# Performance work log

Hardware: AMD Instinct MI355X
Metric: run time of the kernel (lower is better)

The kernel has to match this reference:

```python
import jax, jax.numpy as jnp
import numpy as np

B, N, D = 8, 4096, 6          # clouds, points per cloud, coordinate dim
K = 64                        # max_num_neighbors in radius query
NS1, NS2 = 2048, 512          # fps ratios 0.5 and 0.25
R1, R2 = 0.2, 0.4             # ball-query radii
DIMS = {1: [6, 64, 64, 128], 2: [134, 128, 128, 256], 3: [262, 256, 512, 1024], 4: [1024, 512, 512]}


def setup_inputs():
    key = jax.random.key(0)
    k0, k1, k2 = jax.random.split(key, 3)
    inp = {}
    inp['synapse_cordi'] = jax.random.normal(k0, (B * N, D), jnp.float32)
    inp['batch_index'] = jnp.repeat(jnp.arange(B, dtype=jnp.int32), N)
    inp['weight'] = jax.random.uniform(k1, (B * N,), jnp.float32)
    k = k2
    for i, dims in DIMS.items():
        for j in range(len(dims) - 1):
            k, kw = jax.random.split(k)
            inp[f'w{i}_{j}'] = jax.random.normal(kw, (dims[j], dims[j + 1]), jnp.float32) * (1.0 / float(np.sqrt(dims[j])))
            inp[f'b{i}_{j}'] = jnp.zeros((dims[j + 1],), jnp.float32)
    return inp


def _mlp(x, params):
    # PyG MLP, plain_last=True; batch-norm at default (eval, running stats) is identity
    n = len(params)
    for i, (W, b) in enumerate(params):
        x = x @ W + b
        if i < n - 1:
            x = jax.nn.relu(x)
    return x


def _fps(pos, n_s):
    # farthest point sampling on one cloud [N, D] -> [n_s] indices (deterministic start at 0)
    d0 = jnp.sum((pos - pos[0]) ** 2, axis=-1)
    def step(mind, _):
        nxt = jnp.argmax(mind)
        mind = jnp.minimum(mind, jnp.sum((pos - pos[nxt]) ** 2, axis=-1))
        return mind, nxt
    _, idxs = jax.lax.scan(step, d0, None, length=n_s - 1)
    return jnp.concatenate([jnp.zeros((1,), idxs.dtype), idxs])


def _ball(pos, pos_q, r):
    # radius query: up to K nearest points within r for each query; [n_q,K] idx + validity mask
    d2 = jnp.sum((pos_q[:, None, :] - pos[None, :, :]) ** 2, axis=-1)  # [n_q, N]
    neg = jnp.where(d2 <= r * r, -d2, -jnp.inf)
    vals, nbr = jax.lax.top_k(neg, K)
    return nbr, vals > -jnp.inf


def _sa(x, pos, params, n_s, r):
    # Weight_Sample_Module: fps -> radius -> PointNetConv (gather, MLP, masked max-scatter)
    idx = jax.vmap(lambda p: _fps(p, n_s))(pos)                     # [B, n_s]
    pos_q = jnp.take_along_axis(pos, idx[..., None], axis=1)        # [B, n_s, D]
    nbr, valid = jax.vmap(lambda p, q: _ball(p, q, r))(pos, pos_q)  # [B, n_s, K]
    gather = lambda a: jax.vmap(lambda t, i: t[i])(a, nbr)          # [B, n_s, K, C]
    rel = gather(pos) - pos_q[:, :, None, :]
    feat = rel if x is None else jnp.concatenate([gather(x), rel], axis=-1)
    h = _mlp(feat, params)                                          # [B, n_s, K, C_out]
    h = jnp.where(valid[..., None], h, -jnp.inf)
    return jnp.max(h, axis=2), pos_q                                # max aggregation


def reference(synapse_cordi, batch_index, weight,
              w1_0, b1_0, w1_1, b1_1, w1_2, b1_2,
              w2_0, b2_0, w2_1, b2_1, w2_2, b2_2,
              w3_0, b3_0, w3_1, b3_1, w3_2, b3_2,
              w4_0, b4_0, w4_1, b4_1):
    pos = synapse_cordi.reshape(B, N, D)  # uniform clouds; batch_index = repeat(arange(B), N)
    p1 = [(w1_0, b1_0), (w1_1, b1_1), (w1_2, b1_2)]
    p2 = [(w2_0, b2_0), (w2_1, b2_1), (w2_2, b2_2)]
    p3 = [(w3_0, b3_0), (w3_1, b3_1), (w3_2, b3_2)]
    p4 = [(w4_0, b4_0), (w4_1, b4_1)]
    x1, pos1 = _sa(None, pos, p1, NS1, R1)   # [B, 2048, 128]
    x2, pos2 = _sa(x1, pos1, p2, NS2, R2)    # [B, 512, 256]
    h = _mlp(jnp.concatenate([x2, pos2], axis=-1), p3)  # [B, 512, 1024]
    g = jnp.max(h, axis=1)                   # global max pool -> [B, 1024]
    return _mlp(g, p4)                       # [B, 512]
```

## Files before the change

kernel.cpp:

```cpp
#include <hip/hip_runtime.h>
#include <math.h>

#define B_ 8
#define N_ 4096
#define D_ 6
#define K_ 64
#define NS1_ 2048
#define NS2_ 512

typedef float v2f __attribute__((ext_vector_type(2)));


__device__ __forceinline__ float dist2_rn(const float* __restrict__ a, const float* __restrict__ q) {
    float s = 0.f;
#pragma unroll
    for (int d = 0; d < 6; ++d) {
        float diff = __fsub_rn(a[d], q[d]);
        s = __fadd_rn(s, __fmul_rn(diff, diff));
    }
    return s;
}

__device__ __forceinline__ unsigned mapf(float x) {
    unsigned u = __float_as_uint(x);
    return (u & 0x80000000u) ? ~u : (u | 0x80000000u);
}
__device__ __forceinline__ float unmapf(unsigned u) {
    return __uint_as_float((u & 0x80000000u) ? (u & 0x7FFFFFFFu) : ~u);
}

template <int CTRL>
__device__ __forceinline__ double dppd(double k) {
    int lo = __double2loint(k), hi = __double2hiint(k);
    int nlo = __builtin_amdgcn_update_dpp(lo, lo, CTRL, 0xF, 0xF, false);
    int nhi = __builtin_amdgcn_update_dpp(hi, hi, CTRL, 0xF, 0xF, false);
    return __hiloint2double(nhi, nlo);
}


__device__ __forceinline__ void wait_flag(unsigned* f, int t) {
    if (t == 0) {
        while (__hip_atomic_load(f, __ATOMIC_RELAXED, __HIP_MEMORY_SCOPE_AGENT) == 0u)
            __builtin_amdgcn_s_sleep(32);
        __builtin_amdgcn_fence(__ATOMIC_ACQUIRE, "agent");
    }
    __syncthreads();
}


template <int NP, int NS>
__device__ __forceinline__ void fps_core(float* __restrict__ spos, int* __restrict__ sidx,
                                         double* __restrict__ part, int t) {
#pragma clang fp contract(off)
    constexpr int NT = 256;
    constexpr int P = NP / NT;
    constexpr int HP = P / 2;
    int lane = t & 63, w = t >> 6;

    v2f px2[HP][6];
#pragma unroll
    for (int j = 0; j < HP; ++j)
#pragma unroll
        for (int d = 0; d < 6; ++d) {
            px2[j][d].x = spos[(t + NT * (2 * j)) * 6 + d];
            px2[j][d].y = spos[(t + NT * (2 * j + 1)) * 6 + d];
        }

    float cx[6];
#pragma unroll
    for (int d = 0; d < 6; ++d) cx[d] = spos[d];

    v2f mind2[HP];
    float runv = -1.f;
    int runj = 0;
#pragma unroll
    for (int j = 0; j < HP; ++j) {
        v2f d2 = {0.f, 0.f};
#pragma unroll
        for (int d = 0; d < 6; ++d) {
            v2f df = px2[j][d] - cx[d];
            d2 = d2 + df * df;
        }
        mind2[j] = d2;
        if (d2.x > runv) { runv = d2.x; runj = t + NT * (2 * j); }
        if (d2.y > runv) { runv = d2.y; runj = t + NT * (2 * j + 1); }
    }

    for (int s = 1; s < NS; ++s) {
        double key = __hiloint2double((int)__float_as_uint(runv), (int)(unsigned)(~runj));
        key = fmax(key, dppd<0x111>(key));
        key = fmax(key, dppd<0x112>(key));
        key = fmax(key, dppd<0x114>(key));
        key = fmax(key, dppd<0x118>(key));
        key = fmax(key, dppd<0x142>(key));
        key = fmax(key, dppd<0x143>(key));
        if (lane == 63) part[(s & 1) * 4 + w] = key;
        __syncthreads();
        double kk = part[(s & 1) * 4 + (lane & 3)];
        kk = fmax(kk, dppd<0x111>(kk));
        kk = fmax(kk, dppd<0x112>(kk));
        int nx = ~__builtin_amdgcn_readlane(__double2loint(kk), 3);
        if (t == 0) sidx[s] = nx;

        const float2* sv2 = (const float2*)spos;
        float2 ca = sv2[nx * 3], cb = sv2[nx * 3 + 1], cc = sv2[nx * 3 + 2];
        cx[0] = ca.x; cx[1] = ca.y; cx[2] = cb.x; cx[3] = cb.y; cx[4] = cc.x; cx[5] = cc.y;

        runv = -1.f;
        runj = 0;
#pragma unroll
        for (int j = 0; j < HP; ++j) {
            v2f d2 = {0.f, 0.f};
#pragma unroll
            for (int d = 0; d < 6; ++d) {
                v2f df = px2[j][d] - cx[d];
                d2 = d2 + df * df;
            }
            float mx = fminf(mind2[j].x, d2.x);
            float my = fminf(mind2[j].y, d2.y);
            mind2[j].x = mx;
            mind2[j].y = my;
            if (mx > runv) { runv = mx; runj = t + NT * (2 * j); }
            if (my > runv) { runv = my; runj = t + NT * (2 * j + 1); }
        }
    }
}


template <int NPTS, int S>
__device__ __forceinline__ int ball_scan(const float* __restrict__ sp,
                                         const float* __restrict__ posq,
                                         float r2, int qid, int tid,
                                         float* __restrict__ sd, unsigned short* __restrict__ si) {
    float q[6];
#pragma unroll
    for (int d = 0; d < 6; ++d) q[d] = posq[(size_t)qid * 6 + d];

    int n = 0;
    float thr = INFINITY;
#pragma unroll 4
    for (int j = 0; j < NPTS; ++j) {
        float d2 = dist2_rn(sp + j * 6, q);
        if (d2 <= r2 && (n < K_ || d2 < thr)) {
            int i = (n < K_) ? n : (K_ - 1);
            if (n < K_) ++n;
            while (i > 0 && sd[(i - 1) * S + tid] > d2) {
                sd[i * S + tid] = sd[(i - 1) * S + tid];
                si[i * S + tid] = si[(i - 1) * S + tid];
                --i;
            }
            sd[i * S + tid] = d2;
            si[i * S + tid] = (unsigned short)j;
            if (n == K_) thr = sd[(K_ - 1) * S + tid];
        }
    }
    return n;
}


__global__ __launch_bounds__(256, 1) void stage12_kernel(
        const float* __restrict__ pos, float* __restrict__ pos1, float* __restrict__ pos2,
        float* __restrict__ x1, int* __restrict__ nbr2, int* __restrict__ cnt2,
        unsigned* __restrict__ g, unsigned* flags,
        const float* __restrict__ W1_0, const float* __restrict__ B1_0,
        const float* __restrict__ W1_1, const float* __restrict__ B1_1,
        const float* __restrict__ W1_2, const float* __restrict__ B1_2,
        float r2_1, float r2_2) {
    __shared__ union Smem {
        struct { float spos[N_ * 6]; int sidx[NS1_]; double part[8]; } fps;
        struct { float spos[N_ * 6]; float sd[K_ * 128]; unsigned short si[K_ * 128];
                 unsigned short scnt[128]; } p1;
        struct { float spos1[NS1_ * 6]; float sd2[K_ * 64]; unsigned short si2[K_ * 64]; } b2;
    } sm;
    int t = threadIdx.x;
    int lane = t & 63, w = t >> 6;

    if (blockIdx.x < 8) {
        int b = blockIdx.x;
        float* spos = sm.fps.spos;
        int* sidx = sm.fps.sidx;
        double* part = sm.fps.part;

        {
            const float4* src = (const float4*)(pos + (size_t)b * N_ * 6);
            float4* dst = (float4*)spos;
            for (int e = t; e < N_ * 6 / 4; e += 256) dst[e] = src[e];
        }
        if (t == 0) sidx[0] = 0;
        __syncthreads();

        fps_core<N_, NS1_>(spos, sidx, part, t);
        __syncthreads();

        float smp[NS1_ / 256][6];
#pragma unroll
        for (int i = 0; i < NS1_ / 256; ++i) {
            int s = t + 256 * i;
            int ix = sidx[s];
#pragma unroll
            for (int d = 0; d < 6; ++d) smp[i][d] = spos[ix * 6 + d];
        }
#pragma unroll
        for (int i = 0; i < NS1_ / 256; ++i) {
            int s = t + 256 * i;
#pragma unroll
            for (int d = 0; d < 6; ++d) pos1[((size_t)b * NS1_ + s) * 6 + d] = smp[i][d];
        }
        __syncthreads();
        if (t == 0) {
            __threadfence();
            __hip_atomic_store(&flags[b], 1u, __ATOMIC_RELEASE, __HIP_MEMORY_SCOPE_AGENT);
        }

#pragma unroll
        for (int i = 0; i < NS1_ / 256; ++i) {
            int s = t + 256 * i;
#pragma unroll
            for (int d = 0; d < 6; ++d) spos[s * 6 + d] = smp[i][d];
        }
        for (int e = t; e < 1024; e += 256) g[b * 1024 + e] = 0u;
        if (t == 0) sidx[0] = 0;
        __syncthreads();

        fps_core<NS1_, NS2_>(spos, sidx, part, t);
        __syncthreads();

        for (int s = t; s < NS2_; s += 256) {
            int ix = sidx[s];
#pragma unroll
            for (int d = 0; d < 6; ++d) pos2[((size_t)b * NS2_ + s) * 6 + d] = spos[ix * 6 + d];
        }
        __syncthreads();
        if (t == 0) {
            __threadfence();
            __hip_atomic_store(&flags[8 + b], 1u, __ATOMIC_RELEASE, __HIP_MEMORY_SCOPE_AGENT);
        }
    } else if (blockIdx.x < 8 + 128) {
        int blk = blockIdx.x - 8;
        int b = blk >> 4;
        {
            const float4* src = (const float4*)(pos + (size_t)b * N_ * 6);
            float4* dst = (float4*)sm.p1.spos;
            for (int e = t; e < N_ * 6 / 4; e += 256) dst[e] = src[e];
        }
        __syncthreads();
        wait_flag(&flags[b], t);

        int qbase1 = b * NS1_ + (blk & 15) * 128;
        if (t < 128) {
            int n = ball_scan<N_, 128>(sm.p1.spos, pos1, r2_1, qbase1 + t, t, sm.p1.sd, sm.p1.si);
            sm.p1.scnt[t] = (unsigned short)n;
        }
        __syncthreads();

        for (int qq = 0; qq < 32; ++qq) {
            int lq = w * 32 + qq;
            int qid = qbase1 + lq;
            float q[6];
#pragma unroll
            for (int d = 0; d < 6; ++d) q[d] = pos1[(size_t)qid * 6 + d];
            int c = sm.p1.scnt[lq];
            float m0 = -INFINITY, m1 = -INFINITY;
            for (int n = 0; n < c; ++n) {
                int j = sm.p1.si[n * 128 + lq];
                float rel[6];
#pragma unroll
                for (int d = 0; d < 6; ++d) rel[d] = sm.p1.spos[j * 6 + d] - q[d];
                float a = B1_0[lane];
#pragma unroll
                for (int d = 0; d < 6; ++d) a = fmaf(W1_0[d * 64 + lane], rel[d], a);
                float h1 = fmaxf(a, 0.f);
                float a2 = B1_1[lane];
                for (int k = 0; k < 64; ++k) {
                    float v = __shfl(h1, k, 64);
                    a2 = fmaf(W1_1[k * 64 + lane], v, a2);
                }
                float h2 = fmaxf(a2, 0.f);
                float o0 = B1_2[lane], o1 = B1_2[64 + lane];
                for (int k = 0; k < 64; ++k) {
                    float v = __shfl(h2, k, 64);
                    o0 = fmaf(W1_2[k * 128 + lane], v, o0);
                    o1 = fmaf(W1_2[k * 128 + 64 + lane], v, o1);
                }
                m0 = fmaxf(m0, o0);
                m1 = fmaxf(m1, o1);
            }
            x1[(size_t)qid * 128 + lane] = m0;
            x1[(size_t)qid * 128 + 64 + lane] = m1;
        }
    } else {
        int blk = blockIdx.x - 136;
        int b = blk >> 3;
        wait_flag(&flags[b], t);
        {
            const float4* src = (const float4*)(pos1 + (size_t)b * NS1_ * 6);
            float4* dst = (float4*)sm.b2.spos1;
            for (int e = t; e < NS1_ * 6 / 4; e += 256) dst[e] = src[e];
        }
        __syncthreads();
        wait_flag(&flags[8 + b], t);
        if (t < 64) {
            int qid = blk * 64 + t;
            int n = ball_scan<NS1_, 64>(sm.b2.spos1, pos2, r2_2, qid, t, sm.b2.sd2, sm.b2.si2);
            cnt2[qid] = n;
            for (int i = 0; i < n; ++i) nbr2[(size_t)qid * K_ + i] = (int)sm.b2.si2[i * 64 + t];
        }
    }
}


__global__ __launch_bounds__(256, 1) void sa2_mlp3_kernel(
        const float* __restrict__ pos1, const float* __restrict__ pos2,
        const int* __restrict__ nbr, const int* __restrict__ cnt,
        const float* __restrict__ x1,
        const float* __restrict__ W1, const float* __restrict__ B1,
        const float* __restrict__ W2, const float* __restrict__ B2,
        const float* __restrict__ W3, const float* __restrict__ B3,
        const float* __restrict__ M0, const float* __restrict__ MB0,
        const float* __restrict__ M1, const float* __restrict__ MB1,
        const float* __restrict__ M2, const float* __restrict__ MB2,
        unsigned* __restrict__ g) {
    __shared__ float sx2[16 * 256];
    int lane = threadIdx.x & 63;
    int w = threadIdx.x >> 6;
    int qbase = blockIdx.x * 16;
    int b = qbase >> 9;

    for (int qq = 0; qq < 4; ++qq) {
        int lq = w * 4 + qq;
        int qid = qbase + lq;
        float q[6];
#pragma unroll
        for (int d = 0; d < 6; ++d) q[d] = pos2[(size_t)qid * 6 + d];
        int c = cnt[qid];
        float m0 = -INFINITY, m1 = -INFINITY, m2 = -INFINITY, m3 = -INFINITY;
        for (int n = 0; n < c; ++n) {
            int j = nbr[(size_t)qid * K_ + n];
            size_t row = (size_t)b * NS1_ + j;
            const float* xs = x1 + row * 128;
            float rel[6];
#pragma unroll
            for (int d = 0; d < 6; ++d) rel[d] = pos1[row * 6 + d] - q[d];
            float a0e = B1[lane], a0o = 0.f, a1e = B1[64 + lane], a1o = 0.f;
            for (int k = 0; k < 128; k += 2) {
                float v0 = xs[k], v1 = xs[k + 1];
                a0e = fmaf(W1[k * 128 + lane], v0, a0e);
                a1e = fmaf(W1[k * 128 + 64 + lane], v0, a1e);
                a0o = fmaf(W1[(k + 1) * 128 + lane], v1, a0o);
                a1o = fmaf(W1[(k + 1) * 128 + 64 + lane], v1, a1o);
            }
            float a0 = a0e + a0o, a1 = a1e + a1o;
#pragma unroll
            for (int d = 0; d < 6; ++d) {
                float v = rel[d];
                a0 = fmaf(W1[(128 + d) * 128 + lane], v, a0);
                a1 = fmaf(W1[(128 + d) * 128 + 64 + lane], v, a1);
            }
            float h1a = fmaxf(a0, 0.f), h1b = fmaxf(a1, 0.f);
            float c0 = B2[lane], c1 = B2[64 + lane];
            for (int k = 0; k < 64; ++k) {
                float v = __shfl(h1a, k, 64);
                c0 = fmaf(W2[k * 128 + lane], v, c0);
                c1 = fmaf(W2[k * 128 + 64 + lane], v, c1);
            }
            for (int k = 0; k < 64; ++k) {
                float v = __shfl(h1b, k, 64);
                c0 = fmaf(W2[(64 + k) * 128 + lane], v, c0);
                c1 = fmaf(W2[(64 + k) * 128 + 64 + lane], v, c1);
            }
            float h2a = fmaxf(c0, 0.f), h2b = fmaxf(c1, 0.f);
            float e0 = B3[lane], e1 = B3[64 + lane], e2 = B3[128 + lane], e3 = B3[192 + lane];
            for (int k = 0; k < 64; ++k) {
                float v = __shfl(h2a, k, 64);
                e0 = fmaf(W3[k * 256 + lane], v, e0);
                e1 = fmaf(W3[k * 256 + 64 + lane], v, e1);
                e2 = fmaf(W3[k * 256 + 128 + lane], v, e2);
                e3 = fmaf(W3[k * 256 + 192 + lane], v, e3);
            }
            for (int k = 0; k < 64; ++k) {
                float v = __shfl(h2b, k, 64);
                e0 = fmaf(W3[(64 + k) * 256 + lane], v, e0);
                e1 = fmaf(W3[(64 + k) * 256 + 64 + lane], v, e1);
                e2 = fmaf(W3[(64 + k) * 256 + 128 + lane], v, e2);
                e3 = fmaf(W3[(64 + k) * 256 + 192 + lane], v, e3);
            }
            m0 = fmaxf(m0, e0);
            m1 = fmaxf(m1, e1);
            m2 = fmaxf(m2, e2);
            m3 = fmaxf(m3, e3);
        }
        sx2[lq * 256 + lane] = m0;
        sx2[lq * 256 + 64 + lane] = m1;
        sx2[lq * 256 + 128 + lane] = m2;
        sx2[lq * 256 + 192 + lane] = m3;
    }
    __syncthreads();

    int lq0 = w * 4;
    int qid0 = qbase + lq0;

    float xr[4][4];
#pragma unroll
    for (int q = 0; q < 4; ++q)
#pragma unroll
        for (int j = 0; j < 4; ++j) xr[q][j] = sx2[(lq0 + q) * 256 + j * 64 + lane];

    float a[4][4];
    {
        float4 bv = *(const float4*)&MB0[lane * 4];
#pragma unroll
        for (int q = 0; q < 4; ++q) { a[q][0] = bv.x; a[q][1] = bv.y; a[q][2] = bv.z; a[q][3] = bv.w; }
    }
#pragma unroll
    for (int j = 0; j < 4; ++j) {
        for (int k2 = 0; k2 < 64; ++k2) {
            int k = j * 64 + k2;
            float4 wv = *(const float4*)&M0[(size_t)k * 256 + lane * 4];
#pragma unroll
            for (int q = 0; q < 4; ++q) {
                float v = __shfl(xr[q][j], k2, 64);
                a[q][0] = fmaf(wv.x, v, a[q][0]);
                a[q][1] = fmaf(wv.y, v, a[q][1]);
                a[q][2] = fmaf(wv.z, v, a[q][2]);
                a[q][3] = fmaf(wv.w, v, a[q][3]);
            }
        }
    }
#pragma unroll
    for (int d = 0; d < 6; ++d) {
        float4 wv = *(const float4*)&M0[(size_t)(256 + d) * 256 + lane * 4];
#pragma unroll
        for (int q = 0; q < 4; ++q) {
            float v = pos2[(size_t)(qid0 + q) * 6 + d];
            a[q][0] = fmaf(wv.x, v, a[q][0]);
            a[q][1] = fmaf(wv.y, v, a[q][1]);
            a[q][2] = fmaf(wv.z, v, a[q][2]);
            a[q][3] = fmaf(wv.w, v, a[q][3]);
        }
    }
    float h1[4][4];
#pragma unroll
    for (int q = 0; q < 4; ++q)
#pragma unroll
        for (int u = 0; u < 4; ++u) h1[q][u] = fmaxf(a[q][u], 0.f);

    float c[4][8];
    {
        float4 b0 = *(const float4*)&MB1[lane * 8];
        float4 b1 = *(const float4*)&MB1[lane * 8 + 4];
#pragma unroll
        for (int q = 0; q < 4; ++q) {
            c[q][0] = b0.x; c[q][1] = b0.y; c[q][2] = b0.z; c[q][3] = b0.w;
            c[q][4] = b1.x; c[q][5] = b1.y; c[q][6] = b1.z; c[q][7] = b1.w;
        }
    }
    for (int l = 0; l < 64; ++l) {
#pragma unroll
        for (int r = 0; r < 4; ++r) {
            int k = l * 4 + r;
            float4 w0 = *(const float4*)&M1[(size_t)k * 512 + lane * 8];
            float4 w1 = *(const float4*)&M1[(size_t)k * 512 + lane * 8 + 4];
#pragma unroll
            for (int q = 0; q < 4; ++q) {
                float v = __shfl(h1[q][r], l, 64);
                c[q][0] = fmaf(w0.x, v, c[q][0]);
                c[q][1] = fmaf(w0.y, v, c[q][1]);
                c[q][2] = fmaf(w0.z, v, c[q][2]);
                c[q][3] = fmaf(w0.w, v, c[q][3]);
                c[q][4] = fmaf(w1.x, v, c[q][4]);
                c[q][5] = fmaf(w1.y, v, c[q][5]);
                c[q][6] = fmaf(w1.z, v, c[q][6]);
                c[q][7] = fmaf(w1.w, v, c[q][7]);
            }
        }
    }
    float h2[4][8];
#pragma unroll
    for (int q = 0; q < 4; ++q)
#pragma unroll
        for (int u = 0; u < 8; ++u) h2[q][u] = fmaxf(c[q][u], 0.f);

    float e[4][16];
#pragma unroll
    for (int jj = 0; jj < 4; ++jj) {
        float4 bv = *(const float4*)&MB2[lane * 16 + jj * 4];
#pragma unroll
        for (int q = 0; q < 4; ++q) {
            e[q][jj * 4 + 0] = bv.x; e[q][jj * 4 + 1] = bv.y;
            e[q][jj * 4 + 2] = bv.z; e[q][jj * 4 + 3] = bv.w;
        }
    }
    for (int l = 0; l < 64; ++l) {
#pragma unroll
        for (int r = 0; r < 8; ++r) {
            int k = l * 8 + r;
            const float* wp = &M2[(size_t)k * 1024 + lane * 16];
            float4 w0 = *(const float4*)&wp[0];
            float4 w1 = *(const float4*)&wp[4];
            float4 w2 = *(const float4*)&wp[8];
            float4 w3 = *(const float4*)&wp[12];
#pragma unroll
            for (int q = 0; q < 4; ++q) {
                float v = __shfl(h2[q][r], l, 64);
                e[q][0]  = fmaf(w0.x, v, e[q][0]);
                e[q][1]  = fmaf(w0.y, v, e[q][1]);
                e[q][2]  = fmaf(w0.z, v, e[q][2]);
                e[q][3]  = fmaf(w0.w, v, e[q][3]);
                e[q][4]  = fmaf(w1.x, v, e[q][4]);
                e[q][5]  = fmaf(w1.y, v, e[q][5]);
                e[q][6]  = fmaf(w1.z, v, e[q][6]);
                e[q][7]  = fmaf(w1.w, v, e[q][7]);
                e[q][8]  = fmaf(w2.x, v, e[q][8]);
                e[q][9]  = fmaf(w2.y, v, e[q][9]);
                e[q][10] = fmaf(w2.z, v, e[q][10]);
                e[q][11] = fmaf(w2.w, v, e[q][11]);
                e[q][12] = fmaf(w3.x, v, e[q][12]);
                e[q][13] = fmaf(w3.y, v, e[q][13]);
                e[q][14] = fmaf(w3.z, v, e[q][14]);
                e[q][15] = fmaf(w3.w, v, e[q][15]);
            }
        }
    }
#pragma unroll
    for (int u = 0; u < 16; ++u) {
        float m = fmaxf(fmaxf(e[0][u], e[1][u]), fmaxf(e[2][u], e[3][u]));
        atomicMax(&g[b * 1024 + lane * 16 + u], mapf(m));
    }
}


__global__ __launch_bounds__(512) void mlp4_kernel(const unsigned* __restrict__ g,
                                                   const float* __restrict__ W0, const float* __restrict__ B0,
                                                   const float* __restrict__ W1, const float* __restrict__ B1,
                                                   float* __restrict__ out) {
    int b = blockIdx.x;
    int c = threadIdx.x;
    __shared__ float h[512];
    float a0 = B0[c], a1 = 0.f, a2 = 0.f, a3 = 0.f;
    for (int k = 0; k < 1024; k += 4) {
        float v0 = unmapf(g[b * 1024 + k]);
        float v1 = unmapf(g[b * 1024 + k + 1]);
        float v2 = unmapf(g[b * 1024 + k + 2]);
        float v3 = unmapf(g[b * 1024 + k + 3]);
        a0 = fmaf(v0, W0[k * 512 + c], a0);
        a1 = fmaf(v1, W0[(k + 1) * 512 + c], a1);
        a2 = fmaf(v2, W0[(k + 2) * 512 + c], a2);
        a3 = fmaf(v3, W0[(k + 3) * 512 + c], a3);
    }
    h[c] = fmaxf((a0 + a1) + (a2 + a3), 0.f);
    __syncthreads();
    float o0 = B1[c], o1 = 0.f, o2 = 0.f, o3 = 0.f;
    for (int k = 0; k < 512; k += 4) {
        o0 = fmaf(h[k], W1[k * 512 + c], o0);
        o1 = fmaf(h[k + 1], W1[(k + 1) * 512 + c], o1);
        o2 = fmaf(h[k + 2], W1[(k + 2) * 512 + c], o2);
        o3 = fmaf(h[k + 3], W1[(k + 3) * 512 + c], o3);
    }
    out[(size_t)b * 512 + c] = (o0 + o1) + (o2 + o3);
}


extern "C" void kernel_launch(void* const* d_in, const int* in_sizes, int n_in,
                              void* d_out, int out_size, void* d_ws, size_t ws_size,
                              hipStream_t stream) {
    const float* pos = (const float*)d_in[0];
    const float* w1_0 = (const float*)d_in[3];
    const float* b1_0 = (const float*)d_in[4];
    const float* w1_1 = (const float*)d_in[5];
    const float* b1_1 = (const float*)d_in[6];
    const float* w1_2 = (const float*)d_in[7];
    const float* b1_2 = (const float*)d_in[8];
    const float* w2_0 = (const float*)d_in[9];
    const float* b2_0 = (const float*)d_in[10];
    const float* w2_1 = (const float*)d_in[11];
    const float* b2_1 = (const float*)d_in[12];
    const float* w2_2 = (const float*)d_in[13];
    const float* b2_2 = (const float*)d_in[14];
    const float* w3_0 = (const float*)d_in[15];
    const float* b3_0 = (const float*)d_in[16];
    const float* w3_1 = (const float*)d_in[17];
    const float* b3_1 = (const float*)d_in[18];
    const float* w3_2 = (const float*)d_in[19];
    const float* b3_2 = (const float*)d_in[20];
    const float* w4_0 = (const float*)d_in[21];
    const float* b4_0 = (const float*)d_in[22];
    const float* w4_1 = (const float*)d_in[23];
    const float* b4_1 = (const float*)d_in[24];
    float* out = (float*)d_out;

    char* ws = (char*)d_ws;
    size_t off = 0;
    float* pos1 = (float*)(ws + off);    off += (size_t)B_ * NS1_ * 6 * 4;
    float* pos2 = (float*)(ws + off);    off += (size_t)B_ * NS2_ * 6 * 4;
    float* x1 = (float*)(ws + off);      off += (size_t)B_ * NS1_ * 128 * 4;
    int* nbr2 = (int*)(ws + off);        off += (size_t)B_ * NS2_ * K_ * 4;
    int* cnt2 = (int*)(ws + off);        off += (size_t)B_ * NS2_ * 4;
    unsigned* g = (unsigned*)(ws + off); off += (size_t)B_ * 1024 * 4;
    unsigned* flags = (unsigned*)(ws + off); off += 16 * 4;

    const float r2_1 = (float)(0.2 * 0.2);
    const float r2_2 = (float)(0.4 * 0.4);

    hipMemsetAsync(flags, 0, 16 * 4, stream);

    stage12_kernel<<<200, 256, 0, stream>>>(pos, pos1, pos2, x1, nbr2, cnt2, g, flags,
                                            w1_0, b1_0, w1_1, b1_1, w1_2, b1_2,
                                            r2_1, r2_2);
    sa2_mlp3_kernel<<<(B_ * NS2_) / 16, 256, 0, stream>>>(pos1, pos2, nbr2, cnt2, x1,
                                                          w2_0, b2_0, w2_1, b2_1, w2_2, b2_2,
                                                          w3_0, b3_0, w3_1, b3_1, w3_2, b3_2, g);
    mlp4_kernel<<<B_, 512, 0, stream>>>(g, w4_0, b4_0, w4_1, b4_1, out);
}
```

Before: 2.498 ms.

## Split SA2 conv from MLP3 and stage MLP3 weights in double-buffered LDS

Splits the fused SA2+MLP3 kernel in two. The new SA2 conv kernel handles 4 queries per block without the occupancy-1 bound, so it can launch 1024 blocks instead of 256, and it writes x2 to a global workspace. A separate MLP3 kernel reads x2 and streams the M1/M2 weight rows through double-buffered shared memory, replacing per-lane global loads. This adds an extra kernel launch, an x2 round-trip through global memory, and two block barriers per k-step in MLP3.

```diff
diff --git a/kernel.cpp b/kernel.cpp
--- a/kernel.cpp
+++ b/kernel.cpp
@@ -309,101 +309,103 @@
 }
 
 
-__global__ __launch_bounds__(256, 1) void sa2_mlp3_kernel(
-        const float* __restrict__ pos1, const float* __restrict__ pos2,
-        const int* __restrict__ nbr, const int* __restrict__ cnt,
-        const float* __restrict__ x1,
-        const float* __restrict__ W1, const float* __restrict__ B1,
-        const float* __restrict__ W2, const float* __restrict__ B2,
-        const float* __restrict__ W3, const float* __restrict__ B3,
-        const float* __restrict__ M0, const float* __restrict__ MB0,
-        const float* __restrict__ M1, const float* __restrict__ MB1,
-        const float* __restrict__ M2, const float* __restrict__ MB2,
-        unsigned* __restrict__ g) {
-    __shared__ float sx2[16 * 256];
+__global__ __launch_bounds__(256) void sa2_conv(const float* __restrict__ pos1, const float* __restrict__ posq,
+                                                const int* __restrict__ nbr, const int* __restrict__ cnt,
+                                                const float* __restrict__ x1,
+                                                const float* __restrict__ W1, const float* __restrict__ B1,
+                                                const float* __restrict__ W2, const float* __restrict__ B2,
+                                                const float* __restrict__ W3, const float* __restrict__ B3,
+                                                float* __restrict__ out) {
     int lane = threadIdx.x & 63;
     int w = threadIdx.x >> 6;
-    int qbase = blockIdx.x * 16;
-    int b = qbase >> 9;
-
-    for (int qq = 0; qq < 4; ++qq) {
-        int lq = w * 4 + qq;
-        int qid = qbase + lq;
-        float q[6];
-#pragma unroll
-        for (int d = 0; d < 6; ++d) q[d] = pos2[(size_t)qid * 6 + d];
-        int c = cnt[qid];
-        float m0 = -INFINITY, m1 = -INFINITY, m2 = -INFINITY, m3 = -INFINITY;
-        for (int n = 0; n < c; ++n) {
-            int j = nbr[(size_t)qid * K_ + n];
-            size_t row = (size_t)b * NS1_ + j;
-            const float* xs = x1 + row * 128;
-            float rel[6];
-#pragma unroll
-            for (int d = 0; d < 6; ++d) rel[d] = pos1[row * 6 + d] - q[d];
-            float a0e = B1[lane], a0o = 0.f, a1e = B1[64 + lane], a1o = 0.f;
-            for (int k = 0; k < 128; k += 2) {
-                float v0 = xs[k], v1 = xs[k + 1];
-                a0e = fmaf(W1[k * 128 + lane], v0, a0e);
-                a1e = fmaf(W1[k * 128 + 64 + lane], v0, a1e);
-                a0o = fmaf(W1[(k + 1) * 128 + lane], v1, a0o);
-                a1o = fmaf(W1[(k + 1) * 128 + 64 + lane], v1, a1o);
-            }
-            float a0 = a0e + a0o, a1 = a1e + a1o;
-#pragma unroll
-            for (int d = 0; d < 6; ++d) {
-                float v = rel[d];
-                a0 = fmaf(W1[(128 + d) * 128 + lane], v, a0);
-                a1 = fmaf(W1[(128 + d) * 128 + 64 + lane], v, a1);
-            }
-            float h1a = fmaxf(a0, 0.f), h1b = fmaxf(a1, 0.f);
-            float c0 = B2[lane], c1 = B2[64 + lane];
-            for (int k = 0; k < 64; ++k) {
-                float v = __shfl(h1a, k, 64);
-                c0 = fmaf(W2[k * 128 + lane], v, c0);
-                c1 = fmaf(W2[k * 128 + 64 + lane], v, c1);
-            }
-            for (int k = 0; k < 64; ++k) {
-                float v = __shfl(h1b, k, 64);
-                c0 = fmaf(W2[(64 + k) * 128 + lane], v, c0);
-                c1 = fmaf(W2[(64 + k) * 128 + 64 + lane], v, c1);
-            }
-            float h2a = fmaxf(c0, 0.f), h2b = fmaxf(c1, 0.f);
-            float e0 = B3[lane], e1 = B3[64 + lane], e2 = B3[128 + lane], e3 = B3[192 + lane];
-            for (int k = 0; k < 64; ++k) {
-                float v = __shfl(h2a, k, 64);
-                e0 = fmaf(W3[k * 256 + lane], v, e0);
-                e1 = fmaf(W3[k * 256 + 64 + lane], v, e1);
-                e2 = fmaf(W3[k * 256 + 128 + lane], v, e2);
-                e3 = fmaf(W3[k * 256 + 192 + lane], v, e3);
-            }
-            for (int k = 0; k < 64; ++k) {
-                float v = __shfl(h2b, k, 64);
-                e0 = fmaf(W3[(64 + k) * 256 + lane], v, e0);
-                e1 = fmaf(W3[(64 + k) * 256 + 64 + lane], v, e1);
-                e2 = fmaf(W3[(64 + k) * 256 + 128 + lane], v, e2);
-                e3 = fmaf(W3[(64 + k) * 256 + 192 + lane], v, e3);
-            }
-            m0 = fmaxf(m0, e0);
-            m1 = fmaxf(m1, e1);
-            m2 = fmaxf(m2, e2);
-            m3 = fmaxf(m3, e3);
-        }
-        sx2[lq * 256 + lane] = m0;
-        sx2[lq * 256 + 64 + lane] = m1;
-        sx2[lq * 256 + 128 + lane] = m2;
-        sx2[lq * 256 + 192 + lane] = m3;
-    }
-    __syncthreads();
-
-    int lq0 = w * 4;
-    int qid0 = qbase + lq0;
+    int qid = blockIdx.x * 4 + w;
+    int b = qid / NS2_;
+    float q[6];
+#pragma unroll
+    for (int d = 0; d < 6; ++d) q[d] = posq[(size_t)qid * 6 + d];
+    int c = cnt[qid];
+    float m0 = -INFINITY, m1 = -INFINITY, m2 = -INFINITY, m3 = -INFINITY;
+
+    for (int n = 0; n < c; ++n) {
+        int j = nbr[(size_t)qid * K_ + n];
+        size_t row = (size_t)b * NS1_ + j;
+        const float* xs = x1 + row * 128;
+        float rel[6];
+#pragma unroll
+        for (int d = 0; d < 6; ++d) rel[d] = pos1[row * 6 + d] - q[d];
+        float a0e = B1[lane], a0o = 0.f, a1e = B1[64 + lane], a1o = 0.f;
+        for (int k = 0; k < 128; k += 2) {
+            float v0 = xs[k], v1 = xs[k + 1];
+            a0e = fmaf(W1[k * 128 + lane], v0, a0e);
+            a1e = fmaf(W1[k * 128 + 64 + lane], v0, a1e);
+            a0o = fmaf(W1[(k + 1) * 128 + lane], v1, a0o);
+            a1o = fmaf(W1[(k + 1) * 128 + 64 + lane], v1, a1o);
+        }
+        float a0 = a0e + a0o, a1 = a1e + a1o;
+#pragma unroll
+        for (int d = 0; d < 6; ++d) {
+            float v = rel[d];
+            a0 = fmaf(W1[(128 + d) * 128 + lane], v, a0);
+            a1 = fmaf(W1[(128 + d) * 128 + 64 + lane], v, a1);
+        }
+        float h1a = fmaxf(a0, 0.f), h1b = fmaxf(a1, 0.f);
+        float c0 = B2[lane], c1 = B2[64 + lane];
+        for (int k = 0; k < 64; ++k) {
+            float v = __shfl(h1a, k, 64);
+            c0 = fmaf(W2[k * 128 + lane], v, c0);
+            c1 = fmaf(W2[k * 128 + 64 + lane], v, c1);
+        }
+        for (int k = 0; k < 64; ++k) {
+            float v = __shfl(h1b, k, 64);
+            c0 = fmaf(W2[(64 + k) * 128 + lane], v, c0);
+            c1 = fmaf(W2[(64 + k) * 128 + 64 + lane], v, c1);
+        }
+        float h2a = fmaxf(c0, 0.f), h2b = fmaxf(c1, 0.f);
+        float e0 = B3[lane], e1 = B3[64 + lane], e2 = B3[128 + lane], e3 = B3[192 + lane];
+        for (int k = 0; k < 64; ++k) {
+            float v = __shfl(h2a, k, 64);
+            e0 = fmaf(W3[k * 256 + lane], v, e0);
+            e1 = fmaf(W3[k * 256 + 64 + lane], v, e1);
+            e2 = fmaf(W3[k * 256 + 128 + lane], v, e2);
+            e3 = fmaf(W3[k * 256 + 192 + lane], v, e3);
+        }
+        for (int k = 0; k < 64; ++k) {
+            float v = __shfl(h2b, k, 64);
+            e0 = fmaf(W3[(64 + k) * 256 + lane], v, e0);
+            e1 = fmaf(W3[(64 + k) * 256 + 64 + lane], v, e1);
+            e2 = fmaf(W3[(64 + k) * 256 + 128 + lane], v, e2);
+            e3 = fmaf(W3[(64 + k) * 256 + 192 + lane], v, e3);
+        }
+        m0 = fmaxf(m0, e0);
+        m1 = fmaxf(m1, e1);
+        m2 = fmaxf(m2, e2);
+        m3 = fmaxf(m3, e3);
+    }
+    out[(size_t)qid * 256 + lane] = m0;
+    out[(size_t)qid * 256 + 64 + lane] = m1;
+    out[(size_t)qid * 256 + 128 + lane] = m2;
+    out[(size_t)qid * 256 + 192 + lane] = m3;
+}
+
+
+__global__ __launch_bounds__(256, 1) void mlp3_kernel(const float* __restrict__ x2, const float* __restrict__ pos2,
+                                                      const float* __restrict__ M0, const float* __restrict__ MB0,
+                                                      const float* __restrict__ M1w, const float* __restrict__ MB1,
+                                                      const float* __restrict__ M2w, const float* __restrict__ MB2,
+                                                      unsigned* __restrict__ g) {
+    __shared__ alignas(16) float sM1[2][4 * 512];
+    __shared__ alignas(16) float sM2[2][8 * 1024];
+    int t = threadIdx.x;
+    int lane = t & 63;
+    int w = t >> 6;
+    int qid0 = blockIdx.x * 16 + w * 4;
+    int b = qid0 >> 9;
 
     float xr[4][4];
 #pragma unroll
     for (int q = 0; q < 4; ++q)
 #pragma unroll
-        for (int j = 0; j < 4; ++j) xr[q][j] = sx2[(lq0 + q) * 256 + j * 64 + lane];
+        for (int j = 0; j < 4; ++j) xr[q][j] = x2[(size_t)(qid0 + q) * 256 + j * 64 + lane];
 
     float a[4][4];
     {
@@ -454,12 +456,25 @@
             c[q][4] = b1.x; c[q][5] = b1.y; c[q][6] = b1.z; c[q][7] = b1.w;
         }
     }
+    {
+        const float4* src = (const float4*)M1w;
+        float4* dst = (float4*)sM1[0];
+        dst[t] = src[t];
+        dst[t + 256] = src[t + 256];
+    }
+    __syncthreads();
     for (int l = 0; l < 64; ++l) {
+        int cur = l & 1;
+        float4 rg0, rg1;
+        if (l < 63) {
+            const float4* src = (const float4*)&M1w[(size_t)(l + 1) * 2048];
+            rg0 = src[t];
+            rg1 = src[t + 256];
+        }
 #pragma unroll
         for (int r = 0; r < 4; ++r) {
-            int k = l * 4 + r;
-            float4 w0 = *(const float4*)&M1[(size_t)k * 512 + lane * 8];
-            float4 w1 = *(const float4*)&M1[(size_t)k * 512 + lane * 8 + 4];
+            float4 w0 = *(const float4*)&sM1[cur][r * 512 + lane * 8];
+            float4 w1 = *(const float4*)&sM1[cur][r * 512 + lane * 8 + 4];
 #pragma unroll
             for (int q = 0; q < 4; ++q) {
                 float v = __shfl(h1[q][r], l, 64);
@@ -473,6 +488,13 @@
                 c[q][7] = fmaf(w1.w, v, c[q][7]);
             }
         }
+        __syncthreads();
+        if (l < 63) {
+            float4* dst = (float4*)sM1[cur ^ 1];
+            dst[t] = rg0;
+            dst[t + 256] = rg1;
+        }
+        __syncthreads();
     }
     float h2[4][8];
 #pragma unroll
@@ -490,11 +512,24 @@
             e[q][jj * 4 + 2] = bv.z; e[q][jj * 4 + 3] = bv.w;
         }
     }
+    {
+        const float4* src = (const float4*)M2w;
+        float4* dst = (float4*)sM2[0];
+#pragma unroll
+        for (int i = 0; i < 8; ++i) dst[t + 256 * i] = src[t + 256 * i];
+    }
+    __syncthreads();
     for (int l = 0; l < 64; ++l) {
+        int cur = l & 1;
+        float4 rg[8];
+        if (l < 63) {
+            const float4* src = (const float4*)&M2w[(size_t)(l + 1) * 8192];
+#pragma unroll
+            for (int i = 0; i < 8; ++i) rg[i] = src[t + 256 * i];
+        }
 #pragma unroll
         for (int r = 0; r < 8; ++r) {
-            int k = l * 8 + r;
-            const float* wp = &M2[(size_t)k * 1024 + lane * 16];
+            const float* wp = &sM2[cur][r * 1024 + lane * 16];
             float4 w0 = *(const float4*)&wp[0];
             float4 w1 = *(const float4*)&wp[4];
             float4 w2 = *(const float4*)&wp[8];
@@ -520,6 +555,13 @@
                 e[q][15] = fmaf(w3.w, v, e[q][15]);
             }
         }
+        __syncthreads();
+        if (l < 63) {
+            float4* dst = (float4*)sM2[cur ^ 1];
+#pragma unroll
+            for (int i = 0; i < 8; ++i) dst[t + 256 * i] = rg[i];
+        }
+        __syncthreads();
     }
 #pragma unroll
     for (int u = 0; u < 16; ++u) {
@@ -593,6 +635,7 @@
     float* pos1 = (float*)(ws + off);    off += (size_t)B_ * NS1_ * 6 * 4;
     float* pos2 = (float*)(ws + off);    off += (size_t)B_ * NS2_ * 6 * 4;
     float* x1 = (float*)(ws + off);      off += (size_t)B_ * NS1_ * 128 * 4;
+    float* x2 = (float*)(ws + off);      off += (size_t)B_ * NS2_ * 256 * 4;
     int* nbr2 = (int*)(ws + off);        off += (size_t)B_ * NS2_ * K_ * 4;
     int* cnt2 = (int*)(ws + off);        off += (size_t)B_ * NS2_ * 4;
     unsigned* g = (unsigned*)(ws + off); off += (size_t)B_ * 1024 * 4;
@@ -606,8 +649,9 @@
     stage12_kernel<<<200, 256, 0, stream>>>(pos, pos1, pos2, x1, nbr2, cnt2, g, flags,
                                             w1_0, b1_0, w1_1, b1_1, w1_2, b1_2,
                                             r2_1, r2_2);
-    sa2_mlp3_kernel<<<(B_ * NS2_) / 16, 256, 0, stream>>>(pos1, pos2, nbr2, cnt2, x1,
-                                                          w2_0, b2_0, w2_1, b2_1, w2_2, b2_2,
-                                                          w3_0, b3_0, w3_1, b3_1, w3_2, b3_2, g);
+    sa2_conv<<<(B_ * NS2_) / 4, 256, 0, stream>>>(pos1, pos2, nbr2, cnt2, x1,
+                                                  w2_0, b2_0, w2_1, b2_1, w2_2, b2_2, x2);
+    mlp3_kernel<<<(B_ * NS2_) / 16, 256, 0, stream>>>(x2, pos2, w3_0, b3_0, w3_1, b3_1,
+                                                      w3_2, b3_2, g);
     mlp4_kernel<<<B_, 512, 0, stream>>>(g, w4_0, b4_0, w4_1, b4_1, out);
 }
```

New measurement: 2.518 ms. No clear change (+0.8%).
